# Performance work log

Hardware: AMD Instinct MI355X
Metric: run time of the kernel (lower is better)

## Reference

```python
import jax, jax.numpy as jnp
import numpy as np

D = 256  # out_size / d_model
B, S = 8, 4096


def setup_inputs() -> dict:
    key = jax.random.key(0)
    ks = jax.random.split(key, 10)
    std = 1.0 / np.sqrt(D)
    x = jax.random.normal(ks[0], (B, S, D), dtype=jnp.float32)
    Wq = jax.random.uniform(ks[1], (D, D), jnp.float32, -std, std)
    bq = jax.random.uniform(ks[2], (D,), jnp.float32, -std, std)
    Wk = jax.random.uniform(ks[3], (D, D), jnp.float32, -std, std)
    bk = jax.random.uniform(ks[4], (D,), jnp.float32, -std, std)
    Wv = jax.random.uniform(ks[5], (D, D), jnp.float32, -std, std)
    bv = jax.random.uniform(ks[6], (D,), jnp.float32, -std, std)
    Wo = jax.random.uniform(ks[7], (D, D), jnp.float32, -std, std)
    bo = jax.random.uniform(ks[8], (D,), jnp.float32, -std, std)
    cv = jax.random.normal(ks[9], (D, 1), dtype=jnp.float32)
    return {"x": x, "Wq": Wq, "bq": bq, "Wk": Wk, "bk": bk,
            "Wv": Wv, "bv": bv, "Wo": Wo, "bo": bo, "cv": cv}


def reference(x, Wq, bq, Wk, bk, Wv, bv, Wo, bo, cv):
    # Local single-head attention: separate matmul / softmax / matmul
    q = jnp.einsum('bsd,de->bse', x, Wq) + bq
    k = jnp.einsum('bsd,de->bse', x, Wk) + bk
    v = jnp.einsum('bsd,de->bse', x, Wv) + bv
    scale = jnp.sqrt(jnp.asarray(D, dtype=x.dtype))
    scores = jnp.einsum('bqd,bkd->bqk', q, k) / scale  # [B,S,S]
    attn = jax.nn.softmax(scores, axis=-1)
    ctx = jnp.einsum('bqk,bkd->bqd', attn, v)
    logits = jnp.einsum('bsd,de->bse', ctx, Wo) + bo
    # Global context-vector pooling weights (softmax over sequence dim)
    w = jnp.einsum('bsd,dk->bsk', logits, cv)          # [B,S,1]
    nw = jax.nn.softmax(w, axis=1)
    return logits * nw
```

## Files before the change

kernel.cpp:

```cpp
#include <hip/hip_runtime.h>
#include <math.h>
#include <cstddef>
#include <cstdint>

#define B_ 8
#define S_ 4096
#define D_ 256

typedef __attribute__((ext_vector_type(8))) short short8v;
typedef __attribute__((ext_vector_type(4))) short short4v;
typedef __attribute__((ext_vector_type(4))) float float4v;

__device__ __forceinline__ unsigned short f2bf(float f) {
  unsigned u = __float_as_uint(f);
  return (unsigned short)((u + 0x7FFF + ((u >> 16) & 1)) >> 16);
}
__device__ __forceinline__ float bf2f(unsigned short h) {
  return __uint_as_float((unsigned)h << 16);
}

__global__ __launch_bounds__(256) void wsplit_kernel(
    const float* __restrict__ Wq, const float* __restrict__ Wk,
    const float* __restrict__ Wv, const float* __restrict__ Wo,
    short* __restrict__ wsp) {
  const int mat = blockIdx.x >> 4;
  const int k0  = (blockIdx.x & 15) << 4;
  const float* W = (mat == 0) ? Wq : (mat == 1) ? Wk : (mat == 2) ? Wv : Wo;
  const int n = threadIdx.x;
  short8v h0, h1, l0, l1;
#pragma unroll
  for (int j = 0; j < 8; ++j) {
    float y = W[(size_t)(k0 + j) * 256 + n];
    unsigned short hh = f2bf(y);
    h0[j] = (short)hh; l0[j] = (short)f2bf(y - bf2f(hh));
    y = W[(size_t)(k0 + 8 + j) * 256 + n];
    hh = f2bf(y);
    h1[j] = (short)hh; l1[j] = (short)f2bf(y - bf2f(hh));
  }
  short* dh = wsp + (size_t)mat * 131072 + (size_t)n * 256 + k0;
  short* dl = dh + 65536;
  *(short8v*)(dh + 0) = h0; *(short8v*)(dh + 8) = h1;
  *(short8v*)(dl + 0) = l0; *(short8v*)(dl + 8) = l1;
}

__global__ __launch_bounds__(512, 2) void proj_qkv_mfma(
    const float* __restrict__ x, const short* __restrict__ wsp,
    const float* __restrict__ bq, const float* __restrict__ bk,
    const float* __restrict__ bvv,
    short* __restrict__ qh, short* __restrict__ ql,
    short* __restrict__ kh, short* __restrict__ kl,
    short* __restrict__ vth, short* __restrict__ vtl) {
  __shared__ __align__(16) short sWh[256 * 40];
  __shared__ __align__(16) short sWl[256 * 40];

  const int t    = threadIdx.x;
  const int w    = t >> 6;
  const int lane = t & 63;
  const int m    = lane & 15;
  const int quad = lane >> 4;
  const size_t r0 = (size_t)blockIdx.x * 128;
  const size_t srow = r0 + 16 * w + m;

  short8v xh[8], xl[8];
#pragma unroll
  for (int kk = 0; kk < 8; ++kk) {
    const float* xp = x + srow * 256 + kk * 32 + quad * 8;
    const float4 a = *(const float4*)xp;
    const float4 b2 = *(const float4*)(xp + 4);
    const float v[8] = {a.x, a.y, a.z, a.w, b2.x, b2.y, b2.z, b2.w};
    short8v h, l;
#pragma unroll
    for (int e = 0; e < 8; ++e) {
      const unsigned short hh = f2bf(v[e]);
      h[e] = (short)hh; l[e] = (short)f2bf(v[e] - bf2f(hh));
    }
    xh[kk] = h; xl[kk] = l;
  }

  const int nr   = t >> 1;
  const int kh16 = (t & 1) << 4;
  short8v rh0, rh1, rl0, rl1;
  {
    const short* gh = wsp + (size_t)nr * 256 + kh16;
    const short* gl = gh + 65536;
    rh0 = *(const short8v*)gh;       rh1 = *(const short8v*)(gh + 8);
    rl0 = *(const short8v*)gl;       rl1 = *(const short8v*)(gl + 8);
  }

#pragma unroll
  for (int p = 0; p < 3; ++p) {
    float4v acc[16];
#pragma unroll
    for (int nt = 0; nt < 16; ++nt) acc[nt] = (float4v){0.f, 0.f, 0.f, 0.f};

    for (int kk = 0; kk < 8; ++kk) {
      asm volatile("s_waitcnt lgkmcnt(0)" ::: "memory");
      __builtin_amdgcn_s_barrier();
      asm volatile("" ::: "memory");
      *(short8v*)&sWh[nr * 40 + kh16]     = rh0;
      *(short8v*)&sWh[nr * 40 + kh16 + 8] = rh1;
      *(short8v*)&sWl[nr * 40 + kh16]     = rl0;
      *(short8v*)&sWl[nr * 40 + kh16 + 8] = rl1;
      {
        const int np = (kk < 7) ? p : p + 1;
        const int nk = (kk < 7) ? kk + 1 : 0;
        if (np < 3) {
          const short* gh = wsp + (size_t)np * 131072 +
                            (size_t)nr * 256 + nk * 32 + kh16;
          const short* gl = gh + 65536;
          rh0 = *(const short8v*)gh;   rh1 = *(const short8v*)(gh + 8);
          rl0 = *(const short8v*)gl;   rl1 = *(const short8v*)(gl + 8);
        }
      }
      asm volatile("s_waitcnt lgkmcnt(0)" ::: "memory");
      __builtin_amdgcn_s_barrier();
      asm volatile("" ::: "memory");

      __builtin_amdgcn_s_setprio(1);
#pragma unroll
      for (int nt = 0; nt < 16; ++nt) {
        const short8v wh = *(const short8v*)&sWh[(nt * 16 + m) * 40 + quad * 8];
        const short8v wl = *(const short8v*)&sWl[(nt * 16 + m) * 40 + quad * 8];
        if (p < 2) {
          acc[nt] = __builtin_amdgcn_mfma_f32_16x16x32_bf16(wh, xh[kk], acc[nt], 0, 0, 0);
          acc[nt] = __builtin_amdgcn_mfma_f32_16x16x32_bf16(wh, xl[kk], acc[nt], 0, 0, 0);
          acc[nt] = __builtin_amdgcn_mfma_f32_16x16x32_bf16(wl, xh[kk], acc[nt], 0, 0, 0);
        } else {
          acc[nt] = __builtin_amdgcn_mfma_f32_16x16x32_bf16(xh[kk], wh, acc[nt], 0, 0, 0);
          acc[nt] = __builtin_amdgcn_mfma_f32_16x16x32_bf16(xh[kk], wl, acc[nt], 0, 0, 0);
          acc[nt] = __builtin_amdgcn_mfma_f32_16x16x32_bf16(xl[kk], wh, acc[nt], 0, 0, 0);
        }
      }
      __builtin_amdgcn_s_setprio(0);
    }

    if (p < 2) {
      const float scale = (p == 0) ? 0.0625f : 1.0f;
      short* oh = (p == 0) ? qh : kh;
      short* ol = (p == 0) ? ql : kl;
      const float* bias = (p == 0) ? bq : bk;
#pragma unroll
      for (int nt = 0; nt < 16; ++nt) {
        const float4 bb = *(const float4*)(bias + nt * 16 + quad * 4);
        const float bb4[4] = {bb.x, bb.y, bb.z, bb.w};
        short4v h4, l4;
#pragma unroll
        for (int r = 0; r < 4; ++r) {
          const float y = (acc[nt][r] + bb4[r]) * scale;
          const unsigned short hh = f2bf(y);
          h4[r] = (short)hh; l4[r] = (short)f2bf(y - bf2f(hh));
        }
        *(short4v*)(oh + srow * 256 + nt * 16 + quad * 4) = h4;
        *(short4v*)(ol + srow * 256 + nt * 16 + quad * 4) = l4;
      }
    } else {
      const int bidx = (int)(r0 >> 12);
      const size_t bD = (size_t)bidx * (D_ * (size_t)S_);
      const int sl0 = (int)(r0 & 4095) + 16 * w + quad * 4;
#pragma unroll
      for (int nt = 0; nt < 16; ++nt) {
        const int d = nt * 16 + m;
        const float bn = bvv[d];
        short4v h4, l4;
#pragma unroll
        for (int r = 0; r < 4; ++r) {
          const float y = acc[nt][r] + bn;
          const unsigned short hh = f2bf(y);
          h4[r] = (short)hh; l4[r] = (short)f2bf(y - bf2f(hh));
        }
        *(short4v*)(vth + bD + (size_t)d * S_ + sl0) = h4;
        *(short4v*)(vtl + bD + (size_t)d * S_ + sl0) = l4;
      }
    }
  }
}

__global__ __launch_bounds__(512, 2) void gemm_out_mfma(
    const float* __restrict__ ctx, const short* __restrict__ wsp,
    const float* __restrict__ bo, const float* __restrict__ cv,
    float* __restrict__ out, float* __restrict__ wvec) {
  __shared__ __align__(16) short sWh[256 * 40];
  __shared__ __align__(16) short sWl[256 * 40];

  const int t    = threadIdx.x;
  const int w    = t >> 6;
  const int lane = t & 63;
  const int m    = lane & 15;
  const int quad = lane >> 4;
  const size_t r0 = (size_t)blockIdx.x * 128;
  const size_t srow = r0 + 16 * w + m;
  const short* wbase = wsp + (size_t)3 * 131072;

  short8v ah[8], al[8];
#pragma unroll
  for (int kk = 0; kk < 8; ++kk) {
    const float* xp = ctx + srow * 256 + kk * 32 + quad * 8;
    const float4 a = *(const float4*)xp;
    const float4 b2 = *(const float4*)(xp + 4);
    const float v[8] = {a.x, a.y, a.z, a.w, b2.x, b2.y, b2.z, b2.w};
    short8v h, l;
#pragma unroll
    for (int e = 0; e < 8; ++e) {
      const unsigned short hh = f2bf(v[e]);
      h[e] = (short)hh; l[e] = (short)f2bf(v[e] - bf2f(hh));
    }
    ah[kk] = h; al[kk] = l;
  }

  const int nr   = t >> 1;
  const int kh16 = (t & 1) << 4;
  short8v rh0, rh1, rl0, rl1;
  {
    const short* gh = wbase + (size_t)nr * 256 + kh16;
    const short* gl = gh + 65536;
    rh0 = *(const short8v*)gh;       rh1 = *(const short8v*)(gh + 8);
    rl0 = *(const short8v*)gl;       rl1 = *(const short8v*)(gl + 8);
  }

  float4v acc[16];
#pragma unroll
  for (int nt = 0; nt < 16; ++nt) acc[nt] = (float4v){0.f, 0.f, 0.f, 0.f};

  for (int kk = 0; kk < 8; ++kk) {
    asm volatile("s_waitcnt lgkmcnt(0)" ::: "memory");
    __builtin_amdgcn_s_barrier();
    asm volatile("" ::: "memory");
    *(short8v*)&sWh[nr * 40 + kh16]     = rh0;
    *(short8v*)&sWh[nr * 40 + kh16 + 8] = rh1;
    *(short8v*)&sWl[nr * 40 + kh16]     = rl0;
    *(short8v*)&sWl[nr * 40 + kh16 + 8] = rl1;
    if (kk < 7) {
      const short* gh = wbase + (size_t)nr * 256 + (kk + 1) * 32 + kh16;
      const short* gl = gh + 65536;
      rh0 = *(const short8v*)gh;   rh1 = *(const short8v*)(gh + 8);
      rl0 = *(const short8v*)gl;   rl1 = *(const short8v*)(gl + 8);
    }
    asm volatile("s_waitcnt lgkmcnt(0)" ::: "memory");
    __builtin_amdgcn_s_barrier();
    asm volatile("" ::: "memory");

    __builtin_amdgcn_s_setprio(1);
#pragma unroll
    for (int nt = 0; nt < 16; ++nt) {
      const short8v wh = *(const short8v*)&sWh[(nt * 16 + m) * 40 + quad * 8];
      const short8v wl = *(const short8v*)&sWl[(nt * 16 + m) * 40 + quad * 8];
      acc[nt] = __builtin_amdgcn_mfma_f32_16x16x32_bf16(wh, ah[kk], acc[nt], 0, 0, 0);
      acc[nt] = __builtin_amdgcn_mfma_f32_16x16x32_bf16(wh, al[kk], acc[nt], 0, 0, 0);
      acc[nt] = __builtin_amdgcn_mfma_f32_16x16x32_bf16(wl, ah[kk], acc[nt], 0, 0, 0);
    }
    __builtin_amdgcn_s_setprio(0);
  }

  float wp = 0.f;
  float* orow = out + srow * 256;
#pragma unroll
  for (int nt = 0; nt < 16; ++nt) {
    const float4 bb = *(const float4*)(bo + nt * 16 + quad * 4);
    const float4 cc = *(const float4*)(cv + nt * 16 + quad * 4);
    float4 o;
    o.x = acc[nt][0] + bb.x; o.y = acc[nt][1] + bb.y;
    o.z = acc[nt][2] + bb.z; o.w = acc[nt][3] + bb.w;
    wp += o.x * cc.x + o.y * cc.y + o.z * cc.z + o.w * cc.w;
    *(float4*)(orow + nt * 16 + quad * 4) = o;
  }
  wp += __shfl_xor(wp, 16, 64);
  wp += __shfl_xor(wp, 32, 64);
  if (quad == 0) wvec[srow] = wp;
}

__global__ __launch_bounds__(512, 2) void flash_attn_mfma(
    const short* __restrict__ qh, const short* __restrict__ ql,
    const short* __restrict__ kh, const short* __restrict__ kl,
    const short* __restrict__ vth, const short* __restrict__ vtl,
    float* __restrict__ ctx) {
  __shared__ __align__(16) short sK[16896];
  __shared__ __align__(16) short sPh[8][16][40];
  __shared__ __align__(16) short sPl[8][16][40];
  __shared__ __align__(16) float sAlpha[8][16];
  __shared__ __align__(16) int sF[8];
  __shared__ __align__(16) float sL[128];

  const int t    = threadIdx.x;
  const int w    = t >> 6;
  const int lane = t & 63;
  const int m    = lane & 15;
  const int quad = lane >> 4;
  const int q0   = blockIdx.x * 128;
  const int b    = blockIdx.y;
  const size_t sd = (size_t)b * (S_ * (size_t)D_);
  const size_t bD = (size_t)b * (D_ * (size_t)S_);

  short8v aqh[8], aql[8];
  {
    const size_t row = sd + (size_t)(q0 + 16 * w + m) * D_;
#pragma unroll
    for (int kk = 0; kk < 8; ++kk) {
      const size_t off = row + kk * 32 + quad * 8;
      aqh[kk] = *(const short8v*)(qh + off);
      aql[kk] = *(const short8v*)(ql + off);
    }
  }

  short8v ones;
#pragma unroll
  for (int e = 0; e < 8; ++e) ones[e] = (short)0x3F80;

  float4v acc[8][2];
#pragma unroll
  for (int qt = 0; qt < 8; ++qt) {
    acc[qt][0] = (float4v){0.f, 0.f, 0.f, 0.f};
    acc[qt][1] = (float4v){0.f, 0.f, 0.f, 0.f};
  }
  float4v accl = (float4v){0.f, 0.f, 0.f, 0.f};
  float m_i = -INFINITY;

  const int kr0 = t >> 5;
  const int kc0 = (t & 31) << 3;

  const short* vg0h = vth + bD + (size_t)(((w << 1) + 0) * 16 + m) * S_ + quad * 8;
  const short* vg0l = vtl + bD + (size_t)(((w << 1) + 0) * 16 + m) * S_ + quad * 8;
  const short* vg1h = vth + bD + (size_t)(((w << 1) + 1) * 16 + m) * S_ + quad * 8;
  const short* vg1l = vtl + bD + (size_t)(((w << 1) + 1) * 16 + m) * S_ + quad * 8;

  short8v rKh0, rKh1, rKl0, rKl1;
  short8v rVh0, rVl0, rVh1, rVl1;

  {
    const size_t g0 = sd + (size_t)kr0 * D_ + kc0;
    const size_t g1 = sd + (size_t)(16 + kr0) * D_ + kc0;
    rKh0 = *(const short8v*)(kh + g0);
    rKh1 = *(const short8v*)(kh + g1);
    rKl0 = *(const short8v*)(kl + g0);
    rKl1 = *(const short8v*)(kl + g1);
    rVh0 = *(const short8v*)vg0h;
    rVl0 = *(const short8v*)vg0l;
    rVh1 = *(const short8v*)vg1h;
    rVl1 = *(const short8v*)vg1l;
  }

  for (int jt = 0; jt < 128; ++jt) {
    const int j0 = jt << 5;

    *(short8v*)&sK[kr0 * 264 + kc0]               = rKh0;
    *(short8v*)&sK[(16 + kr0) * 264 + kc0]        = rKh1;
    *(short8v*)&sK[8448 + kr0 * 264 + kc0]        = rKl0;
    *(short8v*)&sK[8448 + (16 + kr0) * 264 + kc0] = rKl1;
    asm volatile("s_waitcnt lgkmcnt(0)" ::: "memory");
    __builtin_amdgcn_s_barrier();
    asm volatile("" ::: "memory");

    float4v s0 = (float4v){0.f, 0.f, 0.f, 0.f};
    float4v s1 = (float4v){0.f, 0.f, 0.f, 0.f};
    __builtin_amdgcn_s_setprio(1);
#pragma unroll
    for (int kk = 0; kk < 8; ++kk) {
      const int co = kk * 32 + quad * 8;
      const short8v bh0 = *(const short8v*)&sK[m * 264 + co];
      const short8v bl0 = *(const short8v*)&sK[8448 + m * 264 + co];
      const short8v bh1 = *(const short8v*)&sK[(16 + m) * 264 + co];
      const short8v bl1 = *(const short8v*)&sK[8448 + (16 + m) * 264 + co];
      s0 = __builtin_amdgcn_mfma_f32_16x16x32_bf16(bh0, aqh[kk], s0, 0, 0, 0);
      s0 = __builtin_amdgcn_mfma_f32_16x16x32_bf16(bh0, aql[kk], s0, 0, 0, 0);
      s0 = __builtin_amdgcn_mfma_f32_16x16x32_bf16(bl0, aqh[kk], s0, 0, 0, 0);
      s1 = __builtin_amdgcn_mfma_f32_16x16x32_bf16(bh1, aqh[kk], s1, 0, 0, 0);
      s1 = __builtin_amdgcn_mfma_f32_16x16x32_bf16(bh1, aql[kk], s1, 0, 0, 0);
      s1 = __builtin_amdgcn_mfma_f32_16x16x32_bf16(bl1, aqh[kk], s1, 0, 0, 0);
    }
    __builtin_amdgcn_s_setprio(0);

    float alpha_p = 1.0f;
    int fired = 0;
    {
      float mx = fmaxf(fmaxf(fmaxf(s0[0], s0[1]), fmaxf(s0[2], s0[3])),
                       fmaxf(fmaxf(s1[0], s1[1]), fmaxf(s1[2], s1[3])));
      mx = fmaxf(mx, __shfl_xor(mx, 16, 64));
      mx = fmaxf(mx, __shfl_xor(mx, 32, 64));
      if (__any(mx > m_i + 8.0f)) {
        const float mnew = fmaxf(m_i, mx);
        alpha_p = __expf(m_i - mnew);
        m_i = mnew;
        fired = 1;
        float al[4];
#pragma unroll
        for (int r = 0; r < 4; ++r) al[r] = __shfl(alpha_p, 20 * quad + r, 64);
#pragma unroll
        for (int r = 0; r < 4; ++r) accl[r] *= al[r];
      }
    }
    if (quad == 0) sAlpha[w][m] = alpha_p;
    if (lane == 0) sF[w] = fired;

    {
      short4v h4a, l4a, h4b, l4b;
#pragma unroll
      for (int r = 0; r < 4; ++r) {
        const float pA = __expf(s0[r] - m_i);
        const unsigned short hA = f2bf(pA);
        h4a[r] = (short)hA; l4a[r] = (short)f2bf(pA - bf2f(hA));
        const float pB = __expf(s1[r] - m_i);
        const unsigned short hB = f2bf(pB);
        h4b[r] = (short)hB; l4b[r] = (short)f2bf(pB - bf2f(hB));
      }
      *(short4v*)&sPh[w][m][4 * quad]      = h4a;
      *(short4v*)&sPh[w][m][16 + 4 * quad] = h4b;
      *(short4v*)&sPl[w][m][4 * quad]      = l4a;
      *(short4v*)&sPl[w][m][16 + 4 * quad] = l4b;
    }

    if (jt < 127) {
      const int j0n = j0 + 32;
      const size_t g0 = sd + (size_t)(j0n + kr0) * D_ + kc0;
      const size_t g1 = sd + (size_t)(j0n + 16 + kr0) * D_ + kc0;
      rKh0 = *(const short8v*)(kh + g0);
      rKh1 = *(const short8v*)(kh + g1);
      rKl0 = *(const short8v*)(kl + g0);
      rKl1 = *(const short8v*)(kl + g1);
    }
    asm volatile("s_waitcnt lgkmcnt(0)" ::: "memory");
    __builtin_amdgcn_s_barrier();
    asm volatile("" ::: "memory");

    {
      const uint4 f0 = *(const uint4*)&sF[0];
      const uint4 f1 = *(const uint4*)&sF[4];
      if (f0.x | f0.y | f0.z | f0.w | f1.x | f1.y | f1.z | f1.w) {
#pragma unroll
        for (int qt = 0; qt < 8; ++qt) {
          const float4 alf = *(const float4*)&sAlpha[qt][quad << 2];
          const float a4[4] = {alf.x, alf.y, alf.z, alf.w};
#pragma unroll
          for (int r = 0; r < 4; ++r) {
            acc[qt][0][r] *= a4[r];
            acc[qt][1][r] *= a4[r];
          }
        }
      }
    }

    __builtin_amdgcn_s_setprio(1);
#pragma unroll
    for (int qt = 0; qt < 8; ++qt) {
      const short8v ph = *(const short8v*)&sPh[qt][m][quad * 8];
      const short8v pl = *(const short8v*)&sPl[qt][m][quad * 8];
      if (qt == w) {
        accl = __builtin_amdgcn_mfma_f32_16x16x32_bf16(ph, ones, accl, 0, 0, 0);
        accl = __builtin_amdgcn_mfma_f32_16x16x32_bf16(pl, ones, accl, 0, 0, 0);
      }
      acc[qt][0] = __builtin_amdgcn_mfma_f32_16x16x32_bf16(ph, rVh0, acc[qt][0], 0, 0, 0);
      acc[qt][0] = __builtin_amdgcn_mfma_f32_16x16x32_bf16(ph, rVl0, acc[qt][0], 0, 0, 0);
      acc[qt][0] = __builtin_amdgcn_mfma_f32_16x16x32_bf16(pl, rVh0, acc[qt][0], 0, 0, 0);
      acc[qt][1] = __builtin_amdgcn_mfma_f32_16x16x32_bf16(ph, rVh1, acc[qt][1], 0, 0, 0);
      acc[qt][1] = __builtin_amdgcn_mfma_f32_16x16x32_bf16(ph, rVl1, acc[qt][1], 0, 0, 0);
      acc[qt][1] = __builtin_amdgcn_mfma_f32_16x16x32_bf16(pl, rVh1, acc[qt][1], 0, 0, 0);
    }
    __builtin_amdgcn_s_setprio(0);

    if (jt < 127) {
      const int j0n = j0 + 32;
      rVh0 = *(const short8v*)(vg0h + j0n);
      rVl0 = *(const short8v*)(vg0l + j0n);
      rVh1 = *(const short8v*)(vg1h + j0n);
      rVl1 = *(const short8v*)(vg1l + j0n);
    }
  }

  if (m == 0) {
#pragma unroll
    for (int r = 0; r < 4; ++r) sL[16 * w + 4 * quad + r] = accl[r];
  }
  __syncthreads();
#pragma unroll
  for (int qt = 0; qt < 8; ++qt) {
    const float4 lf = *(const float4*)&sL[16 * qt + (quad << 2)];
    const float inv4[4] = {1.0f / lf.x, 1.0f / lf.y, 1.0f / lf.z, 1.0f / lf.w};
#pragma unroll
    for (int dtl = 0; dtl < 2; ++dtl) {
      const int d = ((w << 1) + dtl) * 16 + m;
#pragma unroll
      for (int r = 0; r < 4; ++r) {
        ctx[sd + (size_t)(q0 + 16 * qt + 4 * quad + r) * D_ + d] =
            acc[qt][dtl][r] * inv4[r];
      }
    }
  }
}

__global__ __launch_bounds__(256) void softmax_scale_kernel(
    float* __restrict__ out, const float* __restrict__ wv) {
  __shared__ float red[4];
  const int t = threadIdx.x;
  const int wave = t >> 6, lane = t & 63;
  const int b = blockIdx.x >> 8;
  const float* wb = wv + (size_t)b * S_;

  float mx = -INFINITY;
#pragma unroll
  for (int i = 0; i < 16; ++i) mx = fmaxf(mx, wb[t + (i << 8)]);
#pragma unroll
  for (int off = 32; off > 0; off >>= 1) mx = fmaxf(mx, __shfl_xor(mx, off, 64));
  if (lane == 0) red[wave] = mx;
  __syncthreads();
  const float M = fmaxf(fmaxf(red[0], red[1]), fmaxf(red[2], red[3]));
  float sum = 0.f;
#pragma unroll
  for (int i = 0; i < 16; ++i) sum += __expf(wb[t + (i << 8)] - M);
#pragma unroll
  for (int off = 32; off > 0; off >>= 1) sum += __shfl_xor(sum, off, 64);
  __syncthreads();
  if (lane == 0) red[wave] = sum;
  __syncthreads();
  const float inv = 1.0f / (red[0] + red[1] + red[2] + red[3]);

  float4* o4 = (float4*)out;
  const size_t g0 = (size_t)blockIdx.x * 1024 + t;
#pragma unroll
  for (int i = 0; i < 4; ++i) {
    const size_t g = g0 + (size_t)(i << 8);
    const float sc = __expf(wv[g >> 6] - M) * inv;
    float4 vv = o4[g];
    vv.x *= sc; vv.y *= sc; vv.z *= sc; vv.w *= sc;
    o4[g] = vv;
  }
}

extern "C" void kernel_launch(void* const* d_in, const int* in_sizes, int n_in,
                              void* d_out, int out_size, void* d_ws, size_t ws_size,
                              hipStream_t stream) {
  const float* x  = (const float*)d_in[0];
  const float* Wq = (const float*)d_in[1];
  const float* bq = (const float*)d_in[2];
  const float* Wk = (const float*)d_in[3];
  const float* bk = (const float*)d_in[4];
  const float* Wv = (const float*)d_in[5];
  const float* bv = (const float*)d_in[6];
  const float* Wo = (const float*)d_in[7];
  const float* bo = (const float*)d_in[8];
  const float* cv = (const float*)d_in[9];
  float* out = (float*)d_out;

  const size_t N = (size_t)B_ * S_ * D_;
  short* qh  = (short*)d_ws;
  short* ql  = qh + N;
  short* kh  = ql + N;
  short* kl  = kh + N;
  short* vth = kl + N;
  short* vtl = vth + N;
  float* ctx = (float*)(vtl + N);
  float* w   = ctx + N;
  short* wsp = (short*)(w + (size_t)B_ * S_);

  wsplit_kernel<<<64, 256, 0, stream>>>(Wq, Wk, Wv, Wo, wsp);
  proj_qkv_mfma<<<256, 512, 0, stream>>>(x, wsp, bq, bk, bv,
                                         qh, ql, kh, kl, vth, vtl);
  flash_attn_mfma<<<dim3(32, 8), 512, 0, stream>>>(qh, ql, kh, kl, vth, vtl, ctx);
  gemm_out_mfma<<<256, 512, 0, stream>>>(ctx, wsp, bo, cv, out, w);
  softmax_scale_kernel<<<2048, 256, 0, stream>>>(out, w);
}
```

Measured before the change: 550.0 us.

## Halve flash-attention block to 4 waves with 64 queries and 4 D-tiles per wave

Restructures the flash attention kernel from 512-thread blocks over 128 queries to 256-thread blocks over 64 queries, launching 512 blocks instead of 256. Each wave now owns 64 output columns (4 D-tiles) instead of 32, so V registers and accumulators per wave double while the K tile staging is spread over fewer threads (4 loads each). The aim is better CU fill with more blocks across the 256 CUs and cheaper barriers with fewer waves. In exchange K/V are re-read twice as often from global/L2 and register pressure rises.

```diff
diff --git a/kernel.cpp b/kernel.cpp
--- a/kernel.cpp
+++ b/kernel.cpp
@@ -268,24 +268,24 @@
   if (quad == 0) wvec[srow] = wp;
 }
 
-__global__ __launch_bounds__(512, 2) void flash_attn_mfma(
+__global__ __launch_bounds__(256, 2) void flash_attn_mfma(
     const short* __restrict__ qh, const short* __restrict__ ql,
     const short* __restrict__ kh, const short* __restrict__ kl,
     const short* __restrict__ vth, const short* __restrict__ vtl,
     float* __restrict__ ctx) {
   __shared__ __align__(16) short sK[16896];
-  __shared__ __align__(16) short sPh[8][16][40];
-  __shared__ __align__(16) short sPl[8][16][40];
-  __shared__ __align__(16) float sAlpha[8][16];
-  __shared__ __align__(16) int sF[8];
-  __shared__ __align__(16) float sL[128];
+  __shared__ __align__(16) short sPh[4][16][40];
+  __shared__ __align__(16) short sPl[4][16][40];
+  __shared__ __align__(16) float sAlpha[4][16];
+  __shared__ __align__(16) int sF[4];
+  __shared__ __align__(16) float sL[64];
 
   const int t    = threadIdx.x;
   const int w    = t >> 6;
   const int lane = t & 63;
   const int m    = lane & 15;
   const int quad = lane >> 4;
-  const int q0   = blockIdx.x * 128;
+  const int q0   = blockIdx.x * 64;
   const int b    = blockIdx.y;
   const size_t sd = (size_t)b * (S_ * (size_t)D_);
   const size_t bD = (size_t)b * (D_ * (size_t)S_);
@@ -305,46 +305,46 @@
 #pragma unroll
   for (int e = 0; e < 8; ++e) ones[e] = (short)0x3F80;
 
-  float4v acc[8][2];
-#pragma unroll
-  for (int qt = 0; qt < 8; ++qt) {
-    acc[qt][0] = (float4v){0.f, 0.f, 0.f, 0.f};
-    acc[qt][1] = (float4v){0.f, 0.f, 0.f, 0.f};
-  }
+  float4v acc[4][4];
+#pragma unroll
+  for (int qt = 0; qt < 4; ++qt)
+#pragma unroll
+    for (int dtl = 0; dtl < 4; ++dtl)
+      acc[qt][dtl] = (float4v){0.f, 0.f, 0.f, 0.f};
   float4v accl = (float4v){0.f, 0.f, 0.f, 0.f};
   float m_i = -INFINITY;
 
   const int kr0 = t >> 5;
   const int kc0 = (t & 31) << 3;
 
-  const short* vg0h = vth + bD + (size_t)(((w << 1) + 0) * 16 + m) * S_ + quad * 8;
-  const short* vg0l = vtl + bD + (size_t)(((w << 1) + 0) * 16 + m) * S_ + quad * 8;
-  const short* vg1h = vth + bD + (size_t)(((w << 1) + 1) * 16 + m) * S_ + quad * 8;
-  const short* vg1l = vtl + bD + (size_t)(((w << 1) + 1) * 16 + m) * S_ + quad * 8;
-
-  short8v rKh0, rKh1, rKl0, rKl1;
-  short8v rVh0, rVl0, rVh1, rVl1;
+  const short* vgh = vth + bD + (size_t)((4 * w) * 16 + m) * S_ + quad * 8;
+  const short* vgl = vtl + bD + (size_t)((4 * w) * 16 + m) * S_ + quad * 8;
+
+  short8v rKh[4], rKl[4];
+  short8v rVh[4], rVl[4];
 
   {
-    const size_t g0 = sd + (size_t)kr0 * D_ + kc0;
-    const size_t g1 = sd + (size_t)(16 + kr0) * D_ + kc0;
-    rKh0 = *(const short8v*)(kh + g0);
-    rKh1 = *(const short8v*)(kh + g1);
-    rKl0 = *(const short8v*)(kl + g0);
-    rKl1 = *(const short8v*)(kl + g1);
-    rVh0 = *(const short8v*)vg0h;
-    rVl0 = *(const short8v*)vg0l;
-    rVh1 = *(const short8v*)vg1h;
-    rVl1 = *(const short8v*)vg1l;
+#pragma unroll
+    for (int i = 0; i < 4; ++i) {
+      const size_t g = sd + (size_t)(kr0 + 8 * i) * D_ + kc0;
+      rKh[i] = *(const short8v*)(kh + g);
+      rKl[i] = *(const short8v*)(kl + g);
+    }
+#pragma unroll
+    for (int dtl = 0; dtl < 4; ++dtl) {
+      rVh[dtl] = *(const short8v*)(vgh + (size_t)dtl * 16 * S_);
+      rVl[dtl] = *(const short8v*)(vgl + (size_t)dtl * 16 * S_);
+    }
   }
 
   for (int jt = 0; jt < 128; ++jt) {
     const int j0 = jt << 5;
 
-    *(short8v*)&sK[kr0 * 264 + kc0]               = rKh0;
-    *(short8v*)&sK[(16 + kr0) * 264 + kc0]        = rKh1;
-    *(short8v*)&sK[8448 + kr0 * 264 + kc0]        = rKl0;
-    *(short8v*)&sK[8448 + (16 + kr0) * 264 + kc0] = rKl1;
+#pragma unroll
+    for (int i = 0; i < 4; ++i) {
+      *(short8v*)&sK[(kr0 + 8 * i) * 264 + kc0]        = rKh[i];
+      *(short8v*)&sK[8448 + (kr0 + 8 * i) * 264 + kc0] = rKl[i];
+    }
     asm volatile("s_waitcnt lgkmcnt(0)" ::: "memory");
     __builtin_amdgcn_s_barrier();
     asm volatile("" ::: "memory");
@@ -409,58 +409,57 @@
 
     if (jt < 127) {
       const int j0n = j0 + 32;
-      const size_t g0 = sd + (size_t)(j0n + kr0) * D_ + kc0;
-      const size_t g1 = sd + (size_t)(j0n + 16 + kr0) * D_ + kc0;
-      rKh0 = *(const short8v*)(kh + g0);
-      rKh1 = *(const short8v*)(kh + g1);
-      rKl0 = *(const short8v*)(kl + g0);
-      rKl1 = *(const short8v*)(kl + g1);
+#pragma unroll
+      for (int i = 0; i < 4; ++i) {
+        const size_t g = sd + (size_t)(j0n + kr0 + 8 * i) * D_ + kc0;
+        rKh[i] = *(const short8v*)(kh + g);
+        rKl[i] = *(const short8v*)(kl + g);
+      }
     }
     asm volatile("s_waitcnt lgkmcnt(0)" ::: "memory");
     __builtin_amdgcn_s_barrier();
     asm volatile("" ::: "memory");
 
     {
-      const uint4 f0 = *(const uint4*)&sF[0];
-      const uint4 f1 = *(const uint4*)&sF[4];
-      if (f0.x | f0.y | f0.z | f0.w | f1.x | f1.y | f1.z | f1.w) {
-#pragma unroll
-        for (int qt = 0; qt < 8; ++qt) {
+      const int4 ff = *(const int4*)&sF[0];
+      if (ff.x | ff.y | ff.z | ff.w) {
+#pragma unroll
+        for (int qt = 0; qt < 4; ++qt) {
           const float4 alf = *(const float4*)&sAlpha[qt][quad << 2];
           const float a4[4] = {alf.x, alf.y, alf.z, alf.w};
 #pragma unroll
-          for (int r = 0; r < 4; ++r) {
-            acc[qt][0][r] *= a4[r];
-            acc[qt][1][r] *= a4[r];
-          }
+          for (int dtl = 0; dtl < 4; ++dtl)
+#pragma unroll
+            for (int r = 0; r < 4; ++r) acc[qt][dtl][r] *= a4[r];
         }
       }
     }
 
     __builtin_amdgcn_s_setprio(1);
 #pragma unroll
-    for (int qt = 0; qt < 8; ++qt) {
+    for (int qt = 0; qt < 4; ++qt) {
       const short8v ph = *(const short8v*)&sPh[qt][m][quad * 8];
       const short8v pl = *(const short8v*)&sPl[qt][m][quad * 8];
       if (qt == w) {
         accl = __builtin_amdgcn_mfma_f32_16x16x32_bf16(ph, ones, accl, 0, 0, 0);
         accl = __builtin_amdgcn_mfma_f32_16x16x32_bf16(pl, ones, accl, 0, 0, 0);
       }
-      acc[qt][0] = __builtin_amdgcn_mfma_f32_16x16x32_bf16(ph, rVh0, acc[qt][0], 0, 0, 0);
-      acc[qt][0] = __builtin_amdgcn_mfma_f32_16x16x32_bf16(ph, rVl0, acc[qt][0], 0, 0, 0);
-      acc[qt][0] = __builtin_amdgcn_mfma_f32_16x16x32_bf16(pl, rVh0, acc[qt][0], 0, 0, 0);
-      acc[qt][1] = __builtin_amdgcn_mfma_f32_16x16x32_bf16(ph, rVh1, acc[qt][1], 0, 0, 0);
-      acc[qt][1] = __builtin_amdgcn_mfma_f32_16x16x32_bf16(ph, rVl1, acc[qt][1], 0, 0, 0);
-      acc[qt][1] = __builtin_amdgcn_mfma_f32_16x16x32_bf16(pl, rVh1, acc[qt][1], 0, 0, 0);
+#pragma unroll
+      for (int dtl = 0; dtl < 4; ++dtl) {
+        acc[qt][dtl] = __builtin_amdgcn_mfma_f32_16x16x32_bf16(ph, rVh[dtl], acc[qt][dtl], 0, 0, 0);
+        acc[qt][dtl] = __builtin_amdgcn_mfma_f32_16x16x32_bf16(ph, rVl[dtl], acc[qt][dtl], 0, 0, 0);
+        acc[qt][dtl] = __builtin_amdgcn_mfma_f32_16x16x32_bf16(pl, rVh[dtl], acc[qt][dtl], 0, 0, 0);
+      }
     }
     __builtin_amdgcn_s_setprio(0);
 
     if (jt < 127) {
       const int j0n = j0 + 32;
-      rVh0 = *(const short8v*)(vg0h + j0n);
-      rVl0 = *(const short8v*)(vg0l + j0n);
-      rVh1 = *(const short8v*)(vg1h + j0n);
-      rVl1 = *(const short8v*)(vg1l + j0n);
+#pragma unroll
+      for (int dtl = 0; dtl < 4; ++dtl) {
+        rVh[dtl] = *(const short8v*)(vgh + (size_t)dtl * 16 * S_ + j0n);
+        rVl[dtl] = *(const short8v*)(vgl + (size_t)dtl * 16 * S_ + j0n);
+      }
     }
   }
 
@@ -470,12 +469,12 @@
   }
   __syncthreads();
 #pragma unroll
-  for (int qt = 0; qt < 8; ++qt) {
+  for (int qt = 0; qt < 4; ++qt) {
     const float4 lf = *(const float4*)&sL[16 * qt + (quad << 2)];
     const float inv4[4] = {1.0f / lf.x, 1.0f / lf.y, 1.0f / lf.z, 1.0f / lf.w};
 #pragma unroll
-    for (int dtl = 0; dtl < 2; ++dtl) {
-      const int d = ((w << 1) + dtl) * 16 + m;
+    for (int dtl = 0; dtl < 4; ++dtl) {
+      const int d = ((w << 2) + dtl) * 16 + m;
 #pragma unroll
       for (int r = 0; r < 4; ++r) {
         ctx[sd + (size_t)(q0 + 16 * qt + 4 * quad + r) * D_ + d] =
@@ -552,7 +551,7 @@
   wsplit_kernel<<<64, 256, 0, stream>>>(Wq, Wk, Wv, Wo, wsp);
   proj_qkv_mfma<<<256, 512, 0, stream>>>(x, wsp, bq, bk, bv,
                                          qh, ql, kh, kl, vth, vtl);
-  flash_attn_mfma<<<dim3(32, 8), 512, 0, stream>>>(qh, ql, kh, kl, vth, vtl, ctx);
+  flash_attn_mfma<<<dim3(64, 8), 256, 0, stream>>>(qh, ql, kh, kl, vth, vtl, ctx);
   gemm_out_mfma<<<256, 512, 0, stream>>>(ctx, wsp, bo, cv, out, w);
   softmax_scale_kernel<<<2048, 256, 0, stream>>>(out, w);
 }
```

After: 584.1 us. 1.06x slower.
